# Kernel tuning notes

Measured on AMD Instinct MI355X. Metric: run time of the kernel, lower is better.

The kernel has to match this reference:

```python
import jax, jax.numpy as jnp
import numpy as np

DIM_HEAD = 64
LN_EPS = 1e-6  # flax nn.LayerNorm default


def setup_inputs() -> dict:
    key = jax.random.key(0)
    ks = jax.random.split(key, 5)
    B, N, D, H, Dh = 4, 1024, 768, 12, 64
    x = jax.random.normal(ks[0], (B, N, D), dtype=jnp.float32)
    Wq = jax.random.normal(ks[1], (D, H, Dh), dtype=jnp.float32) * (1.0 / np.sqrt(D))
    Wk = jax.random.normal(ks[2], (D, H, Dh), dtype=jnp.float32) * (1.0 / np.sqrt(D))
    Wv = jax.random.normal(ks[3], (D, H, Dh), dtype=jnp.float32) * (1.0 / np.sqrt(D))
    theta = jax.random.normal(ks[4], (H, H), dtype=jnp.float32) * (1.0 / np.sqrt(H))
    ln_scale = jnp.ones((N,), dtype=jnp.float32)
    ln_bias = jnp.zeros((N,), dtype=jnp.float32)
    return {"x": x, "Wq": Wq, "Wk": Wk, "Wv": Wv, "theta": theta,
            "ln_scale": ln_scale, "ln_bias": ln_bias}


def reference(x, Wq, Wk, Wv, theta, ln_scale, ln_bias):
    # x: [B, N, D]; W*: [D, H, Dh]; theta: [H, H]; ln_*: [N]
    q = jnp.einsum('bnd,dhe->bnhe', x, Wq) / jnp.sqrt(jnp.float32(DIM_HEAD))
    k = jnp.einsum('bnd,dhe->bnhe', x, Wk)
    v = jnp.einsum('bnd,dhe->bnhe', x, Wv)
    # attention scores over key axis: [B, H, N, N]
    attn = jnp.einsum('bqhd,bkhd->bhqk', q, k)
    attn = jax.nn.softmax(attn, axis=-1)
    # cross-head theta mixing: 'h i, b h q k -> b i q k'
    attn = jnp.einsum('hi,bhqk->biqk', theta, attn)
    # LayerNorm over last (key) axis with learnable scale/bias of shape [N]
    mean = jnp.mean(attn, axis=-1, keepdims=True)
    var = jnp.mean(jnp.square(attn - mean), axis=-1, keepdims=True)
    attn = (attn - mean) * jax.lax.rsqrt(var + LN_EPS) * ln_scale + ln_bias
    # note: output indexed by k (as in the original source einsum)
    out = jnp.einsum('bhqk,bqhd->bkhd', attn, v)
    B, N, H, Dh = out.shape
    return out.reshape(B, N, H * Dh)
```

## Files before the change

kernel.cpp:

```cpp
#include <hip/hip_runtime.h>

#define NB    4
#define NSEQ  1024
#define DMODEL 768
#define NH    12
#define DH    64

typedef __bf16 bf16x8 __attribute__((ext_vector_type(8)));
typedef float  floatx4 __attribute__((ext_vector_type(4)));
typedef unsigned int u32;

static __device__ __forceinline__ float bf2f(unsigned short u) {
    return __uint_as_float(((unsigned)u) << 16);
}
static __device__ __forceinline__ unsigned short f2bf(float f) {
    unsigned u = __float_as_uint(f);
    u += 0x7FFFu + ((u >> 16) & 1u);
    return (unsigned short)(u >> 16);
}

static __device__ __forceinline__ void gl_lds16(const void* g, void* l) {
    __builtin_amdgcn_global_load_lds(
        (const __attribute__((address_space(1))) unsigned int*)g,
        (__attribute__((address_space(3))) unsigned int*)l, 16, 0, 0);
}

__global__ __launch_bounds__(256) void cast_x(
    const float* __restrict__ x, unsigned short* __restrict__ xb)
{
    const int g = blockIdx.x * 256 + threadIdx.x;
    const size_t base = (size_t)g * 8;
    float4 a = *(const float4*)(x + base);
    float4 b = *(const float4*)(x + base + 4);
    unsigned short o[8];
    o[0] = f2bf(a.x); o[1] = f2bf(a.y); o[2] = f2bf(a.z); o[3] = f2bf(a.w);
    o[4] = f2bf(b.x); o[5] = f2bf(b.y); o[6] = f2bf(b.z); o[7] = f2bf(b.w);
    *(uint4*)(xb + base) = *(uint4*)o;
}

__global__ __launch_bounds__(256) void tr_w(
    const float* __restrict__ Wq, const float* __restrict__ Wk,
    const float* __restrict__ Wv, unsigned short* __restrict__ Wt)
{
    const int z  = blockIdx.z;
    const float* __restrict__ W = (z == 0) ? Wq : (z == 1) ? Wk : Wv;
    const int c0 = blockIdx.x * 64;
    const int k0 = blockIdx.y * 64;
    const int t  = threadIdx.x;

    __shared__ float ls[64][65];

    const int lr = t >> 2;
    #pragma unroll
    for (int j = 0; j < 4; j++) {
        int col = (t & 3) * 16 + j * 4;
        float4 v = *(const float4*)(W + (size_t)(k0 + lr) * DMODEL + c0 + col);
        ls[lr][col + 0] = v.x; ls[lr][col + 1] = v.y;
        ls[lr][col + 2] = v.z; ls[lr][col + 3] = v.w;
    }
    __syncthreads();
    const int lc = t >> 2;
    #pragma unroll
    for (int j = 0; j < 4; j++) {
        int kb = (t & 3) * 16 + j * 4;
        ushort4 o;
        o.x = f2bf(ls[kb + 0][lc]); o.y = f2bf(ls[kb + 1][lc]);
        o.z = f2bf(ls[kb + 2][lc]); o.w = f2bf(ls[kb + 3][lc]);
        *(ushort4*)(Wt + (size_t)z * DMODEL * DMODEL + (size_t)(c0 + lc) * DMODEL + k0 + kb) = o;
    }
}

__global__ __launch_bounds__(256) void qkv_mfma(
    const unsigned short* __restrict__ xb, const unsigned short* __restrict__ Wt,
    unsigned short* __restrict__ Q, unsigned short* __restrict__ K,
    unsigned short* __restrict__ V)
{
    const int z  = blockIdx.z;
    const int r0 = blockIdx.x * 64;
    const int c0 = blockIdx.y * 128;
    const int t    = threadIdx.x;
    const int wave = t >> 6, lane = t & 63;
    const int m = lane & 15, g = lane >> 4;

    const unsigned short* __restrict__ B = Wt + (size_t)z * DMODEL * DMODEL;

    __shared__ __align__(16) char sm[17408];
    unsigned short (*As)[32] = (unsigned short(*)[32])sm;
    unsigned short (*Bs)[32] = (unsigned short(*)[32])(sm + 4096);
    unsigned short (*Po)[136] = (unsigned short(*)[136])sm;

    const int wm = (wave >> 1) * 32;
    const int wn = (wave & 1) * 64;

    floatx4 acc[2][4] = {};

    const unsigned short* ga  = xb + (size_t)(r0 + (t >> 2)) * DMODEL + (t & 3) * 8;
    const unsigned short* gb0 = B  + (size_t)(c0 + (t >> 2)) * DMODEL + (t & 3) * 8;
    const unsigned short* gb1 = B  + (size_t)(c0 + 64 + (t >> 2)) * DMODEL + (t & 3) * 8;
    unsigned short* la  = (unsigned short*)sm + (size_t)t * 8;
    unsigned short* lb0 = (unsigned short*)(sm + 4096) + (size_t)t * 8;
    unsigned short* lb1 = (unsigned short*)(sm + 4096) + (size_t)(t + 256) * 8;

    for (int kk = 0; kk < DMODEL / 32; kk++) {
        gl_lds16(ga  + kk * 32, la);
        gl_lds16(gb0 + kk * 32, lb0);
        gl_lds16(gb1 + kk * 32, lb1);
        __syncthreads();

        bf16x8 af[2], bf[4];
        #pragma unroll
        for (int mt = 0; mt < 2; mt++)
            af[mt] = *(const bf16x8*)&As[wm + mt * 16 + m][g * 8];
        #pragma unroll
        for (int nt = 0; nt < 4; nt++)
            bf[nt] = *(const bf16x8*)&Bs[wn + nt * 16 + m][g * 8];
        #pragma unroll
        for (int mt = 0; mt < 2; mt++)
            #pragma unroll
            for (int nt = 0; nt < 4; nt++)
                acc[mt][nt] = __builtin_amdgcn_mfma_f32_16x16x32_bf16(
                    af[mt], bf[nt], acc[mt][nt], 0, 0, 0);
        __syncthreads();
    }

    const float scale = (z == 0) ? 0.125f : 1.0f;
    #pragma unroll
    for (int mt = 0; mt < 2; mt++) {
        #pragma unroll
        for (int nt = 0; nt < 4; nt++) {
            int rloc = wm + mt * 16 + g * 4;
            int cloc = wn + nt * 16 + m;
            #pragma unroll
            for (int r = 0; r < 4; r++)
                Po[rloc + r][cloc] = f2bf(acc[mt][nt][r] * scale);
        }
    }
    __syncthreads();

    #pragma unroll
    for (int i = 0; i < 4; i++) {
        int ci = t + i * 256;
        int row = ci >> 4, off = (ci & 15) * 8;
        uint4 val = *(uint4*)&Po[row][off];
        if (z == 0) {
            *(uint4*)(Q + (size_t)(r0 + row) * DMODEL + c0 + off) = val;
        } else {
            unsigned short* P = (z == 1) ? K : V;
            int rr = r0 + row;
            int b = rr >> 10, n = rr & 1023;
            int cc = c0 + off;
            int h = cc >> 6, d = cc & 63;
            *(uint4*)(P + (((size_t)b * NH + h) * NSEQ + n) * DH + d) = val;
        }
    }
}

__global__ __launch_bounds__(256) void score_gemm(
    const unsigned short* __restrict__ Q, const unsigned short* __restrict__ K,
    unsigned short* __restrict__ P, float* __restrict__ Lpart)
{
    const int bh = blockIdx.z;
    const int b  = bh / NH, h = bh % NH;
    const int q0 = blockIdx.x * 128;
    const int k0 = blockIdx.y * 128;
    const int t    = threadIdx.x;
    const int wave = t >> 6, lane = t & 63;

    __shared__ __align__(16) char sm[36864];
    unsigned short (*Qs)[72] = (unsigned short(*)[72])sm;
    unsigned short (*Ks)[72] = (unsigned short(*)[72])(sm + 18432);
    unsigned short (*Po)[136] = (unsigned short(*)[136])sm;

    #pragma unroll
    for (int i = 0; i < 4; i++) {
        int c = t + i * 256;
        int row = c >> 3, off = (c & 7) * 8;
        uint4 qa = *(const uint4*)(Q + ((size_t)(b * NSEQ + q0 + row)) * DMODEL + h * DH + off);
        uint4 ka = *(const uint4*)(K + (((size_t)bh) * NSEQ + (k0 + row)) * DH + off);
        *(uint4*)&Qs[row][off] = qa;
        *(uint4*)&Ks[row][off] = ka;
    }
    __syncthreads();

    const int wq = (wave >> 1) * 64, wk2 = (wave & 1) * 64;
    const int m = lane & 15, g = lane >> 4;

    floatx4 acc[4][4] = {};
    #pragma unroll
    for (int ds = 0; ds < 2; ds++) {
        const int dd = ds * 32 + g * 8;
        bf16x8 af[4], bf[4];
        #pragma unroll
        for (int mt = 0; mt < 4; mt++)
            af[mt] = *(const bf16x8*)&Qs[wq + mt * 16 + m][dd];
        #pragma unroll
        for (int nt = 0; nt < 4; nt++)
            bf[nt] = *(const bf16x8*)&Ks[wk2 + nt * 16 + m][dd];
        #pragma unroll
        for (int mt = 0; mt < 4; mt++)
            #pragma unroll
            for (int nt = 0; nt < 4; nt++)
                acc[mt][nt] = __builtin_amdgcn_mfma_f32_16x16x32_bf16(
                    af[mt], bf[nt], acc[mt][nt], 0, 0, 0);
    }

    __syncthreads();
    #pragma unroll
    for (int mt = 0; mt < 4; mt++) {
        #pragma unroll
        for (int nt = 0; nt < 4; nt++) {
            int qloc = wq + mt * 16 + g * 4;
            int kloc = wk2 + nt * 16 + m;
            #pragma unroll
            for (int r = 0; r < 4; r++)
                Po[qloc + r][kloc] = f2bf(__expf(acc[mt][nt][r]));
        }
    }
    __syncthreads();

    if (t < 128) {
        float s = 0.f;
        #pragma unroll
        for (int c8 = 0; c8 < 16; c8++) {
            uint4 w = *(uint4*)&Po[t][c8 * 8];
            const unsigned short* pw = (const unsigned short*)&w;
            #pragma unroll
            for (int j = 0; j < 8; j++) s += bf2f(pw[j]);
        }
        Lpart[((size_t)bh * 8 + blockIdx.y) * NSEQ + q0 + t] = s;
    }

    #pragma unroll
    for (int i = 0; i < 8; i++) {
        int c = t + i * 256;
        int row = c >> 4, off = (c & 15) * 8;
        *(uint4*)(P + (((size_t)bh * NSEQ) + q0 + row) * NSEQ + k0 + off) =
            *(uint4*)&Po[row][off];
    }
}

static __device__ __forceinline__ void reduce12(
    const float* v, float* out12, float* red, int t)
{
    const int lane = t & 63, w = t >> 6;
    #pragma unroll
    for (int h = 0; h < 12; h++) {
        float x = v[h];
        #pragma unroll
        for (int off = 32; off > 0; off >>= 1)
            x += __shfl_down(x, off, 64);
        if (lane == 0) red[w * 12 + h] = x;
    }
    __syncthreads();
    if (t < 12) {
        float x = red[t];
        #pragma unroll
        for (int w2 = 1; w2 < 4; w2++) x += red[w2 * 12 + t];
        out12[t] = x;
    }
    __syncthreads();
}

__global__ __launch_bounds__(256) void mix_fused(
    unsigned short* __restrict__ P, const float* __restrict__ theta,
    const float* __restrict__ Lpart,
    const float* __restrict__ ln_scale, const float* __restrict__ ln_bias)
{
    const int q = blockIdx.x, b = blockIdx.y, t = threadIdx.x;
    __shared__ float th_s[144], red[48], l_l[12], l_s2[12], l_mean[12], l_rstd[12];

    if (t < 12) {
        float s = 0.f;
        #pragma unroll
        for (int kt = 0; kt < 8; kt++)
            s += Lpart[(((size_t)(b * NH + t)) * 8 + kt) * NSEQ + q];
        l_l[t] = s;
        float mean = 0.f;
        #pragma unroll
        for (int h = 0; h < 12; h++) mean += theta[h * 12 + t];
        l_mean[t] = mean * (1.0f / 1024.0f);
    }
    __syncthreads();
    if (t < 144) th_s[t] = theta[t] * (1.0f / l_l[t / 12]);
    __syncthreads();

    unsigned short* Pq = P + ((size_t)b * NH * NSEQ + q) * NSEQ;
    const int k0 = 4 * t;

    float p[12][4];
    #pragma unroll
    for (int h = 0; h < NH; h++) {
        ushort4 u = *(const ushort4*)(Pq + (size_t)h * NSEQ * NSEQ + k0);
        p[h][0] = bf2f(u.x); p[h][1] = bf2f(u.y);
        p[h][2] = bf2f(u.z); p[h][3] = bf2f(u.w);
    }

    float sT2[12];
    #pragma unroll
    for (int i = 0; i < 12; i++) {
        float s0 = 0.f, s1 = 0.f, s2 = 0.f, s3 = 0.f;
        #pragma unroll
        for (int h = 0; h < 12; h++) {
            float th = th_s[h * 12 + i];
            s0 = fmaf(th, p[h][0], s0); s1 = fmaf(th, p[h][1], s1);
            s2 = fmaf(th, p[h][2], s2); s3 = fmaf(th, p[h][3], s3);
        }
        sT2[i] = fmaf(s0, s0, fmaf(s1, s1, fmaf(s2, s2, s3 * s3)));
    }
    reduce12(sT2, l_s2, red, t);
    if (t < 12) {
        float mean = l_mean[t];
        float var  = l_s2[t] * (1.0f / 1024.0f) - mean * mean;
        l_rstd[t] = rsqrtf(var + 1e-6f);
    }
    __syncthreads();

    float4 lsc = *(const float4*)(ln_scale + k0);
    float4 lbs = *(const float4*)(ln_bias + k0);
    #pragma unroll
    for (int i = 0; i < 12; i++) {
        float s0 = 0.f, s1 = 0.f, s2 = 0.f, s3 = 0.f;
        #pragma unroll
        for (int h = 0; h < 12; h++) {
            float th = th_s[h * 12 + i];
            s0 = fmaf(th, p[h][0], s0); s1 = fmaf(th, p[h][1], s1);
            s2 = fmaf(th, p[h][2], s2); s3 = fmaf(th, p[h][3], s3);
        }
        float mm = l_mean[i], rs = l_rstd[i];
        ushort4 o;
        o.x = f2bf(fmaf((s0 - mm) * rs, lsc.x, lbs.x));
        o.y = f2bf(fmaf((s1 - mm) * rs, lsc.y, lbs.y));
        o.z = f2bf(fmaf((s2 - mm) * rs, lsc.z, lbs.z));
        o.w = f2bf(fmaf((s3 - mm) * rs, lsc.w, lbs.w));
        *(ushort4*)(Pq + (size_t)i * NSEQ * NSEQ + k0) = o;
    }
}

__global__ __launch_bounds__(256) void av_mfma(
    const unsigned short* __restrict__ A, const unsigned short* __restrict__ V,
    float* __restrict__ out)
{
    const int b  = blockIdx.z;
    const int i  = blockIdx.y;
    const int k0 = blockIdx.x * 64;
    const int t  = threadIdx.x;
    const int wave = t >> 6, lane = t & 63;
    const int m = lane & 15, g = lane >> 4;

    __shared__ __align__(16) u32 At[64 * 33];
    __shared__ __align__(16) u32 Vt[64 * 33];

    const unsigned short* Ai = A + ((size_t)(b * NH + i)) * NSEQ * NSEQ;
    const unsigned short* Vi = V + ((size_t)(b * NH + i)) * NSEQ * DH;

    const int wk = (wave >> 1) * 32;
    const int wd = (wave & 1) * 32;

    floatx4 acc[2][2] = {};

    for (int q0 = 0; q0 < NSEQ; q0 += 64) {
        ushort4 a0[2], a1[2], v0[2], v1[2];
        #pragma unroll
        for (int l = 0; l < 2; l++) {
            int c = t + l * 256;
            int k4 = (c & 15) * 4;
            int qp = c >> 4;
            a0[l] = *(const ushort4*)(Ai + (size_t)(q0 + 2 * qp)     * NSEQ + k0 + k4);
            a1[l] = *(const ushort4*)(Ai + (size_t)(q0 + 2 * qp + 1) * NSEQ + k0 + k4);
            v0[l] = *(const ushort4*)(Vi + (size_t)(q0 + 2 * qp)     * DH + k4);
            v1[l] = *(const ushort4*)(Vi + (size_t)(q0 + 2 * qp + 1) * DH + k4);
        }
        __syncthreads();
        #pragma unroll
        for (int l = 0; l < 2; l++) {
            int c = t + l * 256;
            int k4 = (c & 15) * 4;
            int qp = c >> 4;
            const unsigned short* pa0 = (const unsigned short*)&a0[l];
            const unsigned short* pa1 = (const unsigned short*)&a1[l];
            const unsigned short* pv0 = (const unsigned short*)&v0[l];
            const unsigned short* pv1 = (const unsigned short*)&v1[l];
            #pragma unroll
            for (int j = 0; j < 4; j++) {
                At[(k4 + j) * 33 + qp] = (u32)pa0[j] | ((u32)pa1[j] << 16);
                Vt[(k4 + j) * 33 + qp] = (u32)pv0[j] | ((u32)pv1[j] << 16);
            }
        }
        __syncthreads();

        #pragma unroll
        for (int ks = 0; ks < 2; ks++) {
            const int qo = ks * 16 + g * 4;
            bf16x8 af[2], bf[2];
            #pragma unroll
            for (int mt = 0; mt < 2; mt++) {
                const u32* r = &At[(wk + mt * 16 + m) * 33 + qo];
                uint4 w; w.x = r[0]; w.y = r[1]; w.z = r[2]; w.w = r[3];
                af[mt] = *(bf16x8*)&w;
            }
            #pragma unroll
            for (int nt = 0; nt < 2; nt++) {
                const u32* r = &Vt[(wd + nt * 16 + m) * 33 + qo];
                uint4 w; w.x = r[0]; w.y = r[1]; w.z = r[2]; w.w = r[3];
                bf[nt] = *(bf16x8*)&w;
            }
            #pragma unroll
            for (int mt = 0; mt < 2; mt++)
                #pragma unroll
                for (int nt = 0; nt < 2; nt++)
                    acc[mt][nt] = __builtin_amdgcn_mfma_f32_16x16x32_bf16(
                        af[mt], bf[nt], acc[mt][nt], 0, 0, 0);
        }
    }

    #pragma unroll
    for (int mt = 0; mt < 2; mt++) {
        #pragma unroll
        for (int nt = 0; nt < 2; nt++) {
            #pragma unroll
            for (int r = 0; r < 4; r++) {
                int k = k0 + wk + mt * 16 + g * 4 + r;
                int d = wd + nt * 16 + m;
                out[((size_t)(b * NSEQ + k)) * DMODEL + i * DH + d] = acc[mt][nt][r];
            }
        }
    }
}

extern "C" void kernel_launch(void* const* d_in, const int* in_sizes, int n_in,
                              void* d_out, int out_size, void* d_ws, size_t ws_size,
                              hipStream_t stream) {
    const float* x     = (const float*)d_in[0];
    const float* Wq    = (const float*)d_in[1];
    const float* Wk    = (const float*)d_in[2];
    const float* Wv    = (const float*)d_in[3];
    const float* theta = (const float*)d_in[4];
    const float* ln_s  = (const float*)d_in[5];
    const float* ln_b  = (const float*)d_in[6];
    float* out = (float*)d_out;

    char* ws = (char*)d_ws;
    const size_t qsz = (size_t)NB * NSEQ * DMODEL * sizeof(unsigned short);
    unsigned short* Q = (unsigned short*)(ws);
    unsigned short* K = (unsigned short*)(ws + qsz);
    unsigned short* V = (unsigned short*)(ws + 2 * qsz);
    unsigned short* P = (unsigned short*)(ws + 3 * qsz);
    unsigned short* xb = P;
    unsigned short* Wt = P + (size_t)NB * NSEQ * DMODEL;

    float* Lpart = out;

    cast_x<<<dim3(NB * NSEQ * DMODEL / 2048), 256, 0, stream>>>(x, xb);
    tr_w<<<dim3(12, 12, 3), 256, 0, stream>>>(Wq, Wk, Wv, Wt);
    qkv_mfma<<<dim3(NB * NSEQ / 64, DMODEL / 128, 3), 256, 0, stream>>>(
        xb, Wt, Q, K, V);
    score_gemm<<<dim3(NSEQ / 128, NSEQ / 128, NB * NH), 256, 0, stream>>>(Q, K, P, Lpart);
    mix_fused<<<dim3(NSEQ, NB), 256, 0, stream>>>(P, theta, Lpart, ln_s, ln_b);
    av_mfma<<<dim3(NSEQ / 64, NH, NB), 256, 0, stream>>>(P, V, out);
}
```

Baseline: 238.3 us.

## Store V transposed and fuse x-cast with weight transpose into one kernel

New measurement: 249.1 us. 1.05x slower.

```diff
diff --git a/kernel.cpp b/kernel.cpp
--- a/kernel.cpp
+++ b/kernel.cpp
@@ -25,28 +25,29 @@
         (__attribute__((address_space(3))) unsigned int*)l, 16, 0, 0);
 }
 
-__global__ __launch_bounds__(256) void cast_x(
-    const float* __restrict__ x, unsigned short* __restrict__ xb)
-{
-    const int g = blockIdx.x * 256 + threadIdx.x;
-    const size_t base = (size_t)g * 8;
-    float4 a = *(const float4*)(x + base);
-    float4 b = *(const float4*)(x + base + 4);
-    unsigned short o[8];
-    o[0] = f2bf(a.x); o[1] = f2bf(a.y); o[2] = f2bf(a.z); o[3] = f2bf(a.w);
-    o[4] = f2bf(b.x); o[5] = f2bf(b.y); o[6] = f2bf(b.z); o[7] = f2bf(b.w);
-    *(uint4*)(xb + base) = *(uint4*)o;
-}
-
-__global__ __launch_bounds__(256) void tr_w(
-    const float* __restrict__ Wq, const float* __restrict__ Wk,
-    const float* __restrict__ Wv, unsigned short* __restrict__ Wt)
-{
-    const int z  = blockIdx.z;
+__global__ __launch_bounds__(256) void prep(
+    const float* __restrict__ x, const float* __restrict__ Wq,
+    const float* __restrict__ Wk, const float* __restrict__ Wv,
+    unsigned short* __restrict__ xb, unsigned short* __restrict__ Wt)
+{
+    const int t = threadIdx.x;
+    if (blockIdx.x < 1536) {
+        const int g = blockIdx.x * 256 + t;
+        const size_t base = (size_t)g * 8;
+        float4 a = *(const float4*)(x + base);
+        float4 b = *(const float4*)(x + base + 4);
+        unsigned short o[8];
+        o[0] = f2bf(a.x); o[1] = f2bf(a.y); o[2] = f2bf(a.z); o[3] = f2bf(a.w);
+        o[4] = f2bf(b.x); o[5] = f2bf(b.y); o[6] = f2bf(b.z); o[7] = f2bf(b.w);
+        *(uint4*)(xb + base) = *(uint4*)o;
+        return;
+    }
+    const int idx = blockIdx.x - 1536;
+    const int z   = idx / 144;
+    const int rem = idx % 144;
+    const int c0  = (rem % 12) * 64;
+    const int k0  = (rem / 12) * 64;
     const float* __restrict__ W = (z == 0) ? Wq : (z == 1) ? Wk : Wv;
-    const int c0 = blockIdx.x * 64;
-    const int k0 = blockIdx.y * 64;
-    const int t  = threadIdx.x;
 
     __shared__ float ls[64][65];
 
@@ -137,20 +138,35 @@
     }
     __syncthreads();
 
-    #pragma unroll
-    for (int i = 0; i < 4; i++) {
-        int ci = t + i * 256;
-        int row = ci >> 4, off = (ci & 15) * 8;
-        uint4 val = *(uint4*)&Po[row][off];
-        if (z == 0) {
-            *(uint4*)(Q + (size_t)(r0 + row) * DMODEL + c0 + off) = val;
-        } else {
-            unsigned short* P = (z == 1) ? K : V;
-            int rr = r0 + row;
-            int b = rr >> 10, n = rr & 1023;
-            int cc = c0 + off;
+    if (z == 2) {
+        const int bb = r0 >> 10, nb = r0 & 1023;
+        #pragma unroll
+        for (int i = 0; i < 4; i++) {
+            int ci = t + i * 256;
+            int col = ci >> 3;
+            int n8  = (ci & 7) * 8;
+            int cc = c0 + col;
             int h = cc >> 6, d = cc & 63;
-            *(uint4*)(P + (((size_t)b * NH + h) * NSEQ + n) * DH + d) = val;
+            unsigned short tmp[8];
+            #pragma unroll
+            for (int j = 0; j < 8; j++) tmp[j] = Po[n8 + j][col];
+            *(uint4*)(V + (((size_t)bb * NH + h) * DH + d) * NSEQ + nb + n8) = *(uint4*)tmp;
+        }
+    } else {
+        #pragma unroll
+        for (int i = 0; i < 4; i++) {
+            int ci = t + i * 256;
+            int row = ci >> 4, off = (ci & 15) * 8;
+            uint4 val = *(uint4*)&Po[row][off];
+            if (z == 0) {
+                *(uint4*)(Q + (size_t)(r0 + row) * DMODEL + c0 + off) = val;
+            } else {
+                int rr = r0 + row;
+                int b = rr >> 10, n = rr & 1023;
+                int cc = c0 + off;
+                int h = cc >> 6, d = cc & 63;
+                *(uint4*)(K + (((size_t)b * NH + h) * NSEQ + n) * DH + d) = val;
+            }
         }
     }
 }
@@ -267,21 +283,21 @@
     const float* __restrict__ ln_scale, const float* __restrict__ ln_bias)
 {
     const int q = blockIdx.x, b = blockIdx.y, t = threadIdx.x;
-    __shared__ float th_s[144], red[48], l_l[12], l_s2[12], l_mean[12], l_rstd[12];
+    __shared__ float th_s[144], red[48], l_s2[12], l_mean[12], l_rstd[12];
 
     if (t < 12) {
         float s = 0.f;
         #pragma unroll
         for (int kt = 0; kt < 8; kt++)
             s += Lpart[(((size_t)(b * NH + t)) * 8 + kt) * NSEQ + q];
-        l_l[t] = s;
+        red[36 + t] = s;
         float mean = 0.f;
         #pragma unroll
         for (int h = 0; h < 12; h++) mean += theta[h * 12 + t];
         l_mean[t] = mean * (1.0f / 1024.0f);
     }
     __syncthreads();
-    if (t < 144) th_s[t] = theta[t] * (1.0f / l_l[t / 12]);
+    if (t < 144) th_s[t] = theta[t] * (1.0f / red[36 + t / 12]);
     __syncthreads();
 
     unsigned short* Pq = P + ((size_t)b * NH * NSEQ + q) * NSEQ;
@@ -337,7 +353,7 @@
 }
 
 __global__ __launch_bounds__(256) void av_mfma(
-    const unsigned short* __restrict__ A, const unsigned short* __restrict__ V,
+    const unsigned short* __restrict__ A, const unsigned short* __restrict__ Vt,
     float* __restrict__ out)
 {
     const int b  = blockIdx.z;
@@ -348,10 +364,10 @@
     const int m = lane & 15, g = lane >> 4;
 
     __shared__ __align__(16) u32 At[64 * 33];
-    __shared__ __align__(16) u32 Vt[64 * 33];
-
-    const unsigned short* Ai = A + ((size_t)(b * NH + i)) * NSEQ * NSEQ;
-    const unsigned short* Vi = V + ((size_t)(b * NH + i)) * NSEQ * DH;
+    __shared__ __align__(16) unsigned short Vs[64 * 72];
+
+    const unsigned short* Ai = A  + ((size_t)(b * NH + i)) * NSEQ * NSEQ;
+    const unsigned short* Vi = Vt + ((size_t)(b * NH + i)) * DH * NSEQ;
 
     const int wk = (wave >> 1) * 32;
     const int wd = (wave & 1) * 32;
@@ -359,7 +375,8 @@
     floatx4 acc[2][2] = {};
 
     for (int q0 = 0; q0 < NSEQ; q0 += 64) {
-        ushort4 a0[2], a1[2], v0[2], v1[2];
+        ushort4 a0[2], a1[2];
+        uint4 vv[2];
         #pragma unroll
         for (int l = 0; l < 2; l++) {
             int c = t + l * 256;
@@ -367,8 +384,8 @@
             int qp = c >> 4;
             a0[l] = *(const ushort4*)(Ai + (size_t)(q0 + 2 * qp)     * NSEQ + k0 + k4);
             a1[l] = *(const ushort4*)(Ai + (size_t)(q0 + 2 * qp + 1) * NSEQ + k0 + k4);
-            v0[l] = *(const ushort4*)(Vi + (size_t)(q0 + 2 * qp)     * DH + k4);
-            v1[l] = *(const ushort4*)(Vi + (size_t)(q0 + 2 * qp + 1) * DH + k4);
+            int vr = c >> 3, vc = (c & 7) * 8;
+            vv[l] = *(const uint4*)(Vi + (size_t)vr * NSEQ + q0 + vc);
         }
         __syncthreads();
         #pragma unroll
@@ -378,32 +395,28 @@
             int qp = c >> 4;
             const unsigned short* pa0 = (const unsigned short*)&a0[l];
             const unsigned short* pa1 = (const unsigned short*)&a1[l];
-            const unsigned short* pv0 = (const unsigned short*)&v0[l];
-            const unsigned short* pv1 = (const unsigned short*)&v1[l];
-            #pragma unroll
-            for (int j = 0; j < 4; j++) {
+            #pragma unroll
+            for (int j = 0; j < 4; j++)
                 At[(k4 + j) * 33 + qp] = (u32)pa0[j] | ((u32)pa1[j] << 16);
-                Vt[(k4 + j) * 33 + qp] = (u32)pv0[j] | ((u32)pv1[j] << 16);
-            }
+            int vr = c >> 3, vc = (c & 7) * 8;
+            *(uint4*)&Vs[vr * 72 + vc] = vv[l];
         }
         __syncthreads();
 
         #pragma unroll
         for (int ks = 0; ks < 2; ks++) {
-            const int qo = ks * 16 + g * 4;
+            const int qoA = ks * 16 + g * 4;
+            const int qoV = ks * 32 + g * 8;
             bf16x8 af[2], bf[2];
             #pragma unroll
             for (int mt = 0; mt < 2; mt++) {
-                const u32* r = &At[(wk + mt * 16 + m) * 33 + qo];
+                const u32* r = &At[(wk + mt * 16 + m) * 33 + qoA];
                 uint4 w; w.x = r[0]; w.y = r[1]; w.z = r[2]; w.w = r[3];
                 af[mt] = *(bf16x8*)&w;
             }
             #pragma unroll
-            for (int nt = 0; nt < 2; nt++) {
-                const u32* r = &Vt[(wd + nt * 16 + m) * 33 + qo];
-                uint4 w; w.x = r[0]; w.y = r[1]; w.z = r[2]; w.w = r[3];
-                bf[nt] = *(bf16x8*)&w;
-            }
+            for (int nt = 0; nt < 2; nt++)
+                bf[nt] = *(const bf16x8*)&Vs[(wd + nt * 16 + m) * 72 + qoV];
             #pragma unroll
             for (int mt = 0; mt < 2; mt++)
                 #pragma unroll
@@ -450,8 +463,7 @@
 
     float* Lpart = out;
 
-    cast_x<<<dim3(NB * NSEQ * DMODEL / 2048), 256, 0, stream>>>(x, xb);
-    tr_w<<<dim3(12, 12, 3), 256, 0, stream>>>(Wq, Wk, Wv, Wt);
+    prep<<<dim3(1536 + 432), 256, 0, stream>>>(x, Wq, Wk, Wv, xb, Wt);
     qkv_mfma<<<dim3(NB * NSEQ / 64, DMODEL / 128, 3), 256, 0, stream>>>(
         xb, Wt, Q, K, V);
     score_gemm<<<dim3(NSEQ / 128, NSEQ / 128, NB * NH), 256, 0, stream>>>(Q, K, P, Lpart);
```
